# Performance work log

Hardware: AMD Instinct MI355X
Metric: run time of the kernel (lower is better)

## Reference

```python
import jax, jax.numpy as jnp
import numpy as np

N = 100000   # n_nodes
E = 1600000  # n_edges
BN_EPS = 1e-5


def setup_inputs() -> dict:
    key = jax.random.key(0)
    ks = jax.random.split(key, 10)
    x = jax.random.normal(ks[0], (N, 20), dtype=jnp.float32)
    edge_index = jax.random.randint(ks[1], (2, E), 0, N, dtype=jnp.int64)
    dims = [(20, 64), (64, 48), (48, 32)]
    inp = {"x": x, "edge_index": edge_index}
    for i, (di, do) in enumerate(dims):
        inp[f"W{i+1}"] = jax.random.normal(ks[2 + i], (di, do), dtype=jnp.float32) / np.sqrt(di)
        inp[f"b{i+1}"] = jnp.zeros((do,), dtype=jnp.float32)
        inp[f"g{i+1}"] = jnp.ones((do,), dtype=jnp.float32)
        inp[f"beta{i+1}"] = jnp.zeros((do,), dtype=jnp.float32)
    return inp


def _gcn_norm(edge_index):
    # add self loops, compute symmetric normalization D^-1/2 (A+I) D^-1/2
    loop = jnp.arange(N, dtype=edge_index.dtype)
    src = jnp.concatenate([edge_index[0], loop])
    dst = jnp.concatenate([edge_index[1], loop])
    deg = jax.ops.segment_sum(jnp.ones_like(src, dtype=jnp.float32), dst, num_segments=N)
    dinv = jax.lax.rsqrt(deg)  # deg >= 1 thanks to self loops
    norm = dinv[src] * dinv[dst]  # [E+N]
    return src, dst, norm


def _gcn_layer(h, src, dst, norm, W, b):
    m = h @ W                                  # [N, out]
    agg = jax.ops.segment_sum(m[src] * norm[:, None], dst, num_segments=N)
    return agg + b


def _batchnorm(x, g, beta):
    mu = jnp.mean(x, axis=0)
    var = jnp.mean(jnp.square(x - mu), axis=0)  # biased, as torch BN training
    return (x - mu) * jax.lax.rsqrt(var + BN_EPS) * g + beta


def reference(x, edge_index, W1, b1, g1, beta1, W2, b2, g2, beta2, W3, b3, g3, beta3):
    src, dst, norm = _gcn_norm(edge_index)
    h = _gcn_layer(x, src, dst, norm, W1, b1)
    h = jax.nn.relu(_batchnorm(h, g1, beta1))   # dropout rate 0 -> identity
    h = _gcn_layer(h, src, dst, norm, W2, b2)
    h = jax.nn.relu(_batchnorm(h, g2, beta2))
    h = _gcn_layer(h, src, dst, norm, W3, b3)
    h = _batchnorm(h, g3, beta3)                # last activation is Identity
    return h
```

## Files before the change

kernel.cpp:

```cpp
#include <hip/hip_runtime.h>


#define NN 100000
#define NE 1600000
constexpr float BN_EPS_F = 1e-5f;

#define BSZ 128
#define NBKT ((NN + BSZ - 1) / BSZ)
#define EC 16384
#define NEB ((NE + EC - 1) / EC)
#define MTOT (NBKT * NEB)
#define CAP 4096


__device__ __forceinline__ unsigned f2bf(float f) {
  union { float f; unsigned u; } v; v.f = f;
  return (v.u + 0x7fffu + ((v.u >> 16) & 1u)) >> 16;
}
__device__ __forceinline__ unsigned pack_bf2(float f0, float f1) {
  return f2bf(f0) | (f2bf(f1) << 16);
}
__device__ __forceinline__ float bf_lo(unsigned u) {
  union { unsigned u; float f; } v; v.u = u << 16; return v.f;
}
__device__ __forceinline__ float bf_hi(unsigned u) {
  union { unsigned u; float f; } v; v.u = u & 0xffff0000u; return v.f;
}


__global__ void hist_pass(const int* __restrict__ dst, int* __restrict__ ph, int e) {
  __shared__ int h[NBKT];
  int tid = threadIdx.x;
  for (int i = tid; i < NBKT; i += 256) h[i] = 0;
  __syncthreads();
  int tbase = blockIdx.x * EC + tid * 64;
#pragma unroll 4
  for (int k = 0; k < 64; k += 4) {
    int i = tbase + k;
    if (i < e) {
      int4 d = *(const int4*)(dst + i);
      atomicAdd(&h[d.x >> 7], 1);
      atomicAdd(&h[d.y >> 7], 1);
      atomicAdd(&h[d.z >> 7], 1);
      atomicAdd(&h[d.w >> 7], 1);
    }
  }
  __syncthreads();
  for (int i = tid; i < NBKT; i += 256) ph[i * NEB + blockIdx.x] = h[i];
}

__global__ void scan_block_sums(const int* __restrict__ data, int* __restrict__ bsums, int n) {
  __shared__ int sd[256];
  int tid = threadIdx.x;
  int base = blockIdx.x * 1024;
  int s = 0;
#pragma unroll
  for (int j = 0; j < 4; j++) {
    int idx = base + tid * 4 + j;
    if (idx < n) s += data[idx];
  }
  sd[tid] = s;
  __syncthreads();
  for (int o = 128; o > 0; o >>= 1) {
    if (tid < o) sd[tid] += sd[tid + o];
    __syncthreads();
  }
  if (tid == 0) bsums[blockIdx.x] = sd[0];
}

__global__ void scan_bsums2(int* __restrict__ bsums, int nb) {
  __shared__ int sd[128];
  int tid = threadIdx.x;
  int v = (tid < nb) ? bsums[tid] : 0;
  sd[tid] = v;
  __syncthreads();
  for (int o = 1; o < 128; o <<= 1) {
    int t = (tid >= o) ? sd[tid - o] : 0;
    __syncthreads();
    sd[tid] += t;
    __syncthreads();
  }
  if (tid < nb) bsums[tid] = sd[tid] - v;
}

__global__ void scan_apply(int* __restrict__ data, const int* __restrict__ bsums, int n) {
  __shared__ int sd[256];
  int tid = threadIdx.x;
  int base = blockIdx.x * 1024;
  int c[4];
  int s = 0;
#pragma unroll
  for (int j = 0; j < 4; j++) {
    int idx = base + tid * 4 + j;
    c[j] = (idx < n) ? data[idx] : 0;
    s += c[j];
  }
  sd[tid] = s;
  __syncthreads();
  for (int o = 1; o < 256; o <<= 1) {
    int t = (tid >= o) ? sd[tid - o] : 0;
    __syncthreads();
    sd[tid] += t;
    __syncthreads();
  }
  int off = bsums[blockIdx.x] + sd[tid] - s;
#pragma unroll
  for (int j = 0; j < 4; j++) {
    int idx = base + tid * 4 + j;
    if (idx < n) {
      data[idx] = off;
      off += c[j];
    }
  }
}

__global__ void bin_pass(const int* __restrict__ src, const int* __restrict__ dst,
                         const int* __restrict__ ph, int* __restrict__ packed, int e) {
  __shared__ int cur[NBKT];
  int tid = threadIdx.x;
  for (int i = tid; i < NBKT; i += 256) cur[i] = ph[i * NEB + blockIdx.x];
  __syncthreads();
  int tbase = blockIdx.x * EC + tid * 64;
#pragma unroll 4
  for (int k = 0; k < 64; k += 4) {
    int i = tbase + k;
    if (i < e) {
      int4 s = *(const int4*)(src + i);
      int4 d = *(const int4*)(dst + i);
      int p0 = atomicAdd(&cur[d.x >> 7], 1);
      int p1 = atomicAdd(&cur[d.y >> 7], 1);
      int p2 = atomicAdd(&cur[d.z >> 7], 1);
      int p3 = atomicAdd(&cur[d.w >> 7], 1);
      packed[p0] = (s.x << 7) | (d.x & 127);
      packed[p1] = (s.y << 7) | (d.y & 127);
      packed[p2] = (s.z << 7) | (d.z & 127);
      packed[p3] = (s.w << 7) | (d.w & 127);
    }
  }
}

__global__ void bucket_finalize(const int* __restrict__ ph, const int* __restrict__ packed,
                                int* __restrict__ rowptr, float* __restrict__ dinv,
                                int* __restrict__ csr_src) {
  __shared__ int eidx[CAP];
  __shared__ int csr_l[CAP];
  __shared__ int ldeg[BSZ], lscan[BSZ], lcur[BSZ];
  int b = blockIdx.x, tid = threadIdx.x;
  int start = ph[b * NEB];
  int end = (b == NBKT - 1) ? NE : ph[(b + 1) * NEB];
  int cnt = end - start;
  if (cnt > CAP) cnt = CAP;
  for (int i = tid; i < cnt; i += 256) eidx[i] = packed[start + i];
  if (tid < BSZ) ldeg[tid] = 0;
  __syncthreads();
  for (int i = tid; i < cnt; i += 256) atomicAdd(&ldeg[eidx[i] & 127], 1);
  __syncthreads();
  if (tid < BSZ) lscan[tid] = ldeg[tid];
  __syncthreads();
  for (int o = 1; o < BSZ; o <<= 1) {
    int t = 0;
    if (tid < BSZ && tid >= o) t = lscan[tid - o];
    __syncthreads();
    if (tid < BSZ) lscan[tid] += t;
    __syncthreads();
  }
  int gn = b * BSZ + tid;
  if (tid < BSZ) {
    int ex = lscan[tid] - ldeg[tid];
    lcur[tid] = ex;
    if (gn < NN) {
      rowptr[gn] = start + ex;
      dinv[gn] = rsqrtf((float)(ldeg[tid] + 1));
    }
  }
  if (b == NBKT - 1 && tid == 0) rowptr[NN] = NE;
  __syncthreads();
  for (int i = tid; i < cnt; i += 256) {
    int pe = eidx[i];
    int pos = atomicAdd(&lcur[pe & 127], 1);
    csr_l[pos] = pe >> 7;
  }
  __syncthreads();
  for (int i = tid; i < cnt; i += 256) csr_src[start + i] = csr_l[i];
}


__global__ void convert_x(const float* __restrict__ x, const float* __restrict__ dinv,
                          unsigned* __restrict__ xb) {
  int t = blockIdx.x * 256 + threadIdx.x;
  if (t >= NN * 16) return;
  int row = t >> 4, i = t & 15;
  unsigned u = 0;
  if (i < 10) {
    float dd = dinv[row];
    float2 f = *(const float2*)(x + row * 20 + 2 * i);
    u = pack_bf2(dd * f.x, dd * f.y);
  }
  xb[t] = u;
}


template <int NU, int S2, int LW, bool STATS>
__launch_bounds__(256)
__global__ void aggregate_bf(const unsigned* __restrict__ mb, const int* __restrict__ rowptr,
                             const int* __restrict__ csr_src, const float* __restrict__ dinv,
                             const float* __restrict__ bias, float* __restrict__ out,
                             float* __restrict__ gsum) {
  constexpr int NPB = 256 / LW;
  constexpr int OS = 2 * LW;
  __shared__ float2 ssum[256], ssq[256];
  int tid = threadIdx.x;
  int sub = tid / LW, lane = tid % LW;
  int cl = (lane < NU) ? lane : lane - NU;
  int d = blockIdx.x * NPB + sub;
  int start = rowptr[d], end = rowptr[d + 1];
  unsigned su = mb[(size_t)d * S2 + cl];
  float acc0 = bf_lo(su), acc1 = bf_hi(su);
  int j = start;
  int aligned = (start + 3) & ~3;
  int pe = aligned < end ? aligned : end;
  for (; j < pe; j++) {
    unsigned u = mb[(size_t)csr_src[j] * S2 + cl];
    acc0 += bf_lo(u); acc1 += bf_hi(u);
  }
  for (; j + 16 <= end; j += 16) {
    int4 s0 = *(const int4*)(csr_src + j);
    int4 s1 = *(const int4*)(csr_src + j + 4);
    int4 s2 = *(const int4*)(csr_src + j + 8);
    int4 s3 = *(const int4*)(csr_src + j + 12);
    unsigned u0 = mb[(size_t)s0.x * S2 + cl], u1 = mb[(size_t)s0.y * S2 + cl];
    unsigned u2 = mb[(size_t)s0.z * S2 + cl], u3 = mb[(size_t)s0.w * S2 + cl];
    unsigned u4 = mb[(size_t)s1.x * S2 + cl], u5 = mb[(size_t)s1.y * S2 + cl];
    unsigned u6 = mb[(size_t)s1.z * S2 + cl], u7 = mb[(size_t)s1.w * S2 + cl];
    unsigned u8 = mb[(size_t)s2.x * S2 + cl], u9 = mb[(size_t)s2.y * S2 + cl];
    unsigned ua = mb[(size_t)s2.z * S2 + cl], ub = mb[(size_t)s2.w * S2 + cl];
    unsigned uc = mb[(size_t)s3.x * S2 + cl], ud = mb[(size_t)s3.y * S2 + cl];
    unsigned ue = mb[(size_t)s3.z * S2 + cl], uf = mb[(size_t)s3.w * S2 + cl];
    acc0 += bf_lo(u0) + bf_lo(u1) + bf_lo(u2) + bf_lo(u3);
    acc1 += bf_hi(u0) + bf_hi(u1) + bf_hi(u2) + bf_hi(u3);
    acc0 += bf_lo(u4) + bf_lo(u5) + bf_lo(u6) + bf_lo(u7);
    acc1 += bf_hi(u4) + bf_hi(u5) + bf_hi(u6) + bf_hi(u7);
    acc0 += bf_lo(u8) + bf_lo(u9) + bf_lo(ua) + bf_lo(ub);
    acc1 += bf_hi(u8) + bf_hi(u9) + bf_hi(ua) + bf_hi(ub);
    acc0 += bf_lo(uc) + bf_lo(ud) + bf_lo(ue) + bf_lo(uf);
    acc1 += bf_hi(uc) + bf_hi(ud) + bf_hi(ue) + bf_hi(uf);
  }
  for (; j + 4 <= end; j += 4) {
    int4 s0 = *(const int4*)(csr_src + j);
    unsigned u0 = mb[(size_t)s0.x * S2 + cl], u1 = mb[(size_t)s0.y * S2 + cl];
    unsigned u2 = mb[(size_t)s0.z * S2 + cl], u3 = mb[(size_t)s0.w * S2 + cl];
    acc0 += bf_lo(u0) + bf_lo(u1) + bf_lo(u2) + bf_lo(u3);
    acc1 += bf_hi(u0) + bf_hi(u1) + bf_hi(u2) + bf_hi(u3);
  }
  for (; j < end; j++) {
    unsigned u = mb[(size_t)csr_src[j] * S2 + cl];
    acc0 += bf_lo(u); acc1 += bf_hi(u);
  }
  float dd = dinv[d];
  float v0 = dd * acc0, v1 = dd * acc1;
  if (bias) { v0 += bias[2 * cl]; v1 += bias[2 * cl + 1]; }
  if (lane >= NU) { v0 = 0.f; v1 = 0.f; }
  *(float2*)(out + (size_t)d * OS + 2 * lane) = make_float2(v0, v1);
  if (STATS) {
    ssum[tid] = make_float2(v0, v1);
    ssq[tid] = make_float2(v0 * v0, v1 * v1);
    __syncthreads();
    if (tid < LW) {
      float s0 = 0.f, s1 = 0.f, q0 = 0.f, q1 = 0.f;
#pragma unroll
      for (int k = 0; k < NPB; k++) {
        float2 a = ssum[k * LW + tid];
        float2 b = ssq[k * LW + tid];
        s0 += a.x; s1 += a.y; q0 += b.x; q1 += b.y;
      }
      if (tid < NU) {
        float* gs = gsum + (blockIdx.x & 31) * 128;
        atomicAdd(&gs[2 * tid], s0);
        atomicAdd(&gs[2 * tid + 1], s1);
        atomicAdd(&gs[64 + 2 * tid], q0);
        atomicAdd(&gs[64 + 2 * tid + 1], q1);
      }
    }
  }
}


__launch_bounds__(256)
__global__ void gemm1_stats(const float* __restrict__ h, const float* __restrict__ W,
                            const float* __restrict__ bias, float* __restrict__ out,
                            float* __restrict__ gsum) {
  __shared__ float Wl[20 * 64];
  __shared__ float Hl[8][32];
  __shared__ float2 ssum[256], ssq[256];
  int tid = threadIdx.x;
  int row0 = blockIdx.x * 8;
  for (int i = tid; i < 20 * 64; i += 256) Wl[i] = W[i];
  {
    int r = tid >> 5, k = tid & 31;
    Hl[r][k] = h[(size_t)(row0 + r) * 32 + k];
  }
  __syncthreads();
  int r = tid >> 5, c2 = tid & 31;
  float acc0 = bias[2 * c2], acc1 = bias[2 * c2 + 1];
#pragma unroll
  for (int k = 0; k < 20; k++) {
    float a = Hl[r][k];
    acc0 = fmaf(a, Wl[k * 64 + 2 * c2], acc0);
    acc1 = fmaf(a, Wl[k * 64 + 2 * c2 + 1], acc1);
  }
  *(float2*)(out + (size_t)(row0 + r) * 64 + 2 * c2) = make_float2(acc0, acc1);
  ssum[tid] = make_float2(acc0, acc1);
  ssq[tid] = make_float2(acc0 * acc0, acc1 * acc1);
  __syncthreads();
  if (tid < 32) {
    float s0 = 0.f, s1 = 0.f, q0 = 0.f, q1 = 0.f;
#pragma unroll
    for (int k = 0; k < 8; k++) {
      float2 a = ssum[k * 32 + tid];
      float2 b = ssq[k * 32 + tid];
      s0 += a.x; s1 += a.y; q0 += b.x; q1 += b.y;
    }
    float* gs = gsum + (blockIdx.x & 31) * 128;
    atomicAdd(&gs[2 * tid], s0);
    atomicAdd(&gs[2 * tid + 1], s1);
    atomicAdd(&gs[64 + 2 * tid], q0);
    atomicAdd(&gs[64 + 2 * tid + 1], q1);
  }
}


template <int K, int HS, int C, int S2, int R>
__launch_bounds__(256)
__global__ void gemm_bf(const float* __restrict__ h, const float* __restrict__ W,
                        const float* __restrict__ scale, const float* __restrict__ shift,
                        const float* __restrict__ dinv, unsigned* __restrict__ out) {
  __shared__ float Wl[K * C];
  __shared__ float Hl[R][K];
  int tid = threadIdx.x;
  int row0 = blockIdx.x * R;
  for (int i = tid; i < K * C; i += 256) Wl[i] = W[i];
  for (int i = tid; i < R * K; i += 256) {
    int r = i / K, k = i % K;
    float v = h[(size_t)(row0 + r) * HS + k];
    v = fmaf(v, scale[k], shift[k]);
    Hl[r][k] = fmaxf(v, 0.f);
  }
  __syncthreads();
  int r = tid / S2, c2 = tid % S2;
  unsigned u = 0;
  if (2 * c2 < C) {
    float acc0 = 0.f, acc1 = 0.f;
#pragma unroll
    for (int k = 0; k < K; k++) {
      float a = Hl[r][k];
      acc0 = fmaf(a, Wl[k * C + 2 * c2], acc0);
      acc1 = fmaf(a, Wl[k * C + 2 * c2 + 1], acc1);
    }
    float dd = dinv[row0 + r];
    u = pack_bf2(dd * acc0, dd * acc1);
  }
  out[(size_t)(row0 + r) * S2 + c2] = u;
}


__global__ void bn_finalize(const float* __restrict__ gsum, const float* __restrict__ g,
                            const float* __restrict__ beta, float* __restrict__ scale,
                            float* __restrict__ shift, int C, float invn) {
  int i = threadIdx.x;
  if (i < C) {
    float s = 0.f, q = 0.f;
    for (int b = 0; b < 32; b++) {
      s += gsum[b * 128 + i];
      q += gsum[b * 128 + 64 + i];
    }
    float mean = s * invn;
    float var = q * invn - mean * mean;
    var = fmaxf(var, 0.f);
    float inv = rsqrtf(var + BN_EPS_F);
    float sc = g[i] * inv;
    scale[i] = sc;
    shift[i] = beta[i] - mean * sc;
  }
}

__global__ void bn_apply_out(const float* __restrict__ h, const float* __restrict__ scale,
                             const float* __restrict__ shift, float* __restrict__ out, int total) {
  int i = blockIdx.x * blockDim.x + threadIdx.x;
  if (i < total) {
    int c = i & 31;
    out[i] = h[i] * scale[c] + shift[c];
  }
}


extern "C" void kernel_launch(void* const* d_in, const int* in_sizes, int n_in,
                              void* d_out, int out_size, void* d_ws, size_t ws_size,
                              hipStream_t stream) {
  const float* x = (const float*)d_in[0];
  const int* ei = (const int*)d_in[1];
  const float* W1 = (const float*)d_in[2];
  const float* b1 = (const float*)d_in[3];
  const float* g1 = (const float*)d_in[4];
  const float* be1 = (const float*)d_in[5];
  const float* W2 = (const float*)d_in[6];
  const float* b2 = (const float*)d_in[7];
  const float* g2 = (const float*)d_in[8];
  const float* be2 = (const float*)d_in[9];
  const float* W3 = (const float*)d_in[10];
  const float* b3 = (const float*)d_in[11];
  const float* g3 = (const float*)d_in[12];
  const float* be3 = (const float*)d_in[13];
  float* out = (float*)d_out;

  const int* src = ei;
  const int* dst = ei + NE;

  char* ws = (char*)d_ws;
  size_t off = 0;
  auto alloc = [&](size_t bytes) -> void* {
    void* p = ws + off;
    off += bytes;
    off = (off + 255) & ~(size_t)255;
    return p;
  };
  int* ph = (int*)alloc((size_t)MTOT * 4);
  int* bsums = (int*)alloc(128 * 4);
  int* packed = (int*)alloc((size_t)NE * 4);
  int* rowptr = (int*)alloc((NN + 1) * 4);
  int* csr_src = (int*)alloc((size_t)NE * 4);
  float* dinv = (float*)alloc(NN * 4);
  float* gsum = (float*)alloc(3 * 32 * 128 * 4);
  float* scsh = (float*)alloc(3 * 128 * 4);
  float* bufP = (float*)alloc((size_t)NN * 32 * 4);
  float* bufQ = (float*)alloc((size_t)NN * 64 * 4);
  float* bufR = (float*)alloc((size_t)NN * 32 * 4);

  unsigned* xb = (unsigned*)bufR;
  float* aggx = bufP;
  float* h1 = bufQ;
  unsigned* m2b = (unsigned*)bufP;
  float* h2 = bufQ;
  unsigned* m3b = (unsigned*)bufP;
  float* h3 = bufR;

  hipMemsetAsync(gsum, 0, 3 * 32 * 128 * 4, stream);

  const int nscan = (MTOT + 1023) / 1024;
  hist_pass<<<NEB, 256, 0, stream>>>(dst, ph, NE);
  scan_block_sums<<<nscan, 256, 0, stream>>>(ph, bsums, MTOT);
  scan_bsums2<<<1, 128, 0, stream>>>(bsums, nscan);
  scan_apply<<<nscan, 256, 0, stream>>>(ph, bsums, MTOT);
  bin_pass<<<NEB, 256, 0, stream>>>(src, dst, ph, packed, NE);
  bucket_finalize<<<NBKT, 256, 0, stream>>>(ph, packed, rowptr, dinv, csr_src);
  convert_x<<<NN * 16 / 256, 256, 0, stream>>>(x, dinv, xb);

  const float invn = 1.f / (float)NN;

  aggregate_bf<10, 16, 16, false><<<NN / 16, 256, 0, stream>>>(xb, rowptr, csr_src, dinv,
                                                               nullptr, aggx, nullptr);
  gemm1_stats<<<NN / 8, 256, 0, stream>>>(aggx, W1, b1, h1, gsum);
  bn_finalize<<<1, 64, 0, stream>>>(gsum, g1, be1, scsh + 0, scsh + 64, 64, invn);

  gemm_bf<64, 64, 48, 32, 8><<<NN / 8, 256, 0, stream>>>(h1, W2, scsh + 0, scsh + 64, dinv, m2b);
  aggregate_bf<24, 32, 32, true><<<NN / 8, 256, 0, stream>>>(m2b, rowptr, csr_src, dinv, b2, h2,
                                                             gsum + 4096);
  bn_finalize<<<1, 64, 0, stream>>>(gsum + 4096, g2, be2, scsh + 128, scsh + 192, 48, invn);

  gemm_bf<48, 64, 32, 16, 16><<<NN / 16, 256, 0, stream>>>(h2, W3, scsh + 128, scsh + 192, dinv, m3b);
  aggregate_bf<16, 16, 16, true><<<NN / 16, 256, 0, stream>>>(m3b, rowptr, csr_src, dinv, b3, h3,
                                                              gsum + 8192);
  bn_finalize<<<1, 64, 0, stream>>>(gsum + 8192, g3, be3, scsh + 256, scsh + 320, 32, invn);

  bn_apply_out<<<(NN * 32 + 255) / 256, 256, 0, stream>>>(h3, scsh + 256, scsh + 320, out, NN * 32);
}
```

Baseline: 359.9 us.

## Fuse x conversion into CSR build and store intermediates as bf16

Folds the x-to-bf16 scaling into bucket_finalize, which removes one launch and one reread of dinv. Intermediate activations (aggregated x, h1, h2) are now stored as packed bf16 rather than fp32, which shrinks memory traffic between the GEMM and aggregation stages. The templated aggregate and gemm kernels become specialized versions, and layer 2 packs 48 channels as 12 uint2 lanes per row instead of 24 padded lanes of 32. The cost is extra bf16 rounding on intermediates and on the values that feed the BatchNorm statistics, plus a larger workspace from separate buffers.

```diff
diff --git a/kernel.cpp b/kernel.cpp
--- a/kernel.cpp
+++ b/kernel.cpp
@@ -140,11 +140,13 @@
 }
 
 __global__ void bucket_finalize(const int* __restrict__ ph, const int* __restrict__ packed,
-                                int* __restrict__ rowptr, float* __restrict__ dinv,
-                                int* __restrict__ csr_src) {
+                                const float* __restrict__ x, int* __restrict__ rowptr,
+                                float* __restrict__ dinv, int* __restrict__ csr_src,
+                                unsigned* __restrict__ xb) {
   __shared__ int eidx[CAP];
   __shared__ int csr_l[CAP];
   __shared__ int ldeg[BSZ], lscan[BSZ], lcur[BSZ];
+  __shared__ float ldinv[BSZ];
   int b = blockIdx.x, tid = threadIdx.x;
   int start = ph[b * NEB];
   int end = (b == NBKT - 1) ? NE : ph[(b + 1) * NEB];
@@ -168,9 +170,11 @@
   if (tid < BSZ) {
     int ex = lscan[tid] - ldeg[tid];
     lcur[tid] = ex;
+    float dv = rsqrtf((float)(ldeg[tid] + 1));
+    ldinv[tid] = dv;
     if (gn < NN) {
       rowptr[gn] = start + ex;
-      dinv[gn] = rsqrtf((float)(ldeg[tid] + 1));
+      dinv[gn] = dv;
     }
   }
   if (b == NBKT - 1 && tid == 0) rowptr[NN] = NE;
@@ -182,45 +186,38 @@
   }
   __syncthreads();
   for (int i = tid; i < cnt; i += 256) csr_src[start + i] = csr_l[i];
-}
-
-
-__global__ void convert_x(const float* __restrict__ x, const float* __restrict__ dinv,
-                          unsigned* __restrict__ xb) {
-  int t = blockIdx.x * 256 + threadIdx.x;
-  if (t >= NN * 16) return;
-  int row = t >> 4, i = t & 15;
-  unsigned u = 0;
-  if (i < 10) {
-    float dd = dinv[row];
-    float2 f = *(const float2*)(x + row * 20 + 2 * i);
-    u = pack_bf2(dd * f.x, dd * f.y);
-  }
-  xb[t] = u;
-}
-
-
-template <int NU, int S2, int LW, bool STATS>
+  for (int i = tid; i < BSZ * 16; i += 256) {
+    int nl = i >> 4, j = i & 15;
+    int g2 = b * BSZ + nl;
+    if (g2 < NN) {
+      unsigned u = 0;
+      if (j < 10) {
+        float2 f = *(const float2*)(x + (size_t)g2 * 20 + 2 * j);
+        float dd = ldinv[nl];
+        u = pack_bf2(dd * f.x, dd * f.y);
+      }
+      xb[(size_t)g2 * 16 + j] = u;
+    }
+  }
+}
+
+
 __launch_bounds__(256)
-__global__ void aggregate_bf(const unsigned* __restrict__ mb, const int* __restrict__ rowptr,
-                             const int* __restrict__ csr_src, const float* __restrict__ dinv,
-                             const float* __restrict__ bias, float* __restrict__ out,
-                             float* __restrict__ gsum) {
-  constexpr int NPB = 256 / LW;
-  constexpr int OS = 2 * LW;
-  __shared__ float2 ssum[256], ssq[256];
-  int tid = threadIdx.x;
-  int sub = tid / LW, lane = tid % LW;
-  int cl = (lane < NU) ? lane : lane - NU;
-  int d = blockIdx.x * NPB + sub;
+__global__ void aggregate_x(const unsigned* __restrict__ mb, const int* __restrict__ rowptr,
+                            const int* __restrict__ csr_src, const float* __restrict__ dinv,
+                            unsigned* __restrict__ out) {
+  int tid = threadIdx.x;
+  int sub = tid >> 4, lane = tid & 15;
+  int cl = (lane < 10) ? lane : lane - 10;
+  int d = blockIdx.x * 16 + sub;
   int start = rowptr[d], end = rowptr[d + 1];
-  unsigned su = mb[(size_t)d * S2 + cl];
+  unsigned su = mb[(size_t)d * 16 + cl];
   float acc0 = bf_lo(su), acc1 = bf_hi(su);
   int j = start;
   int aligned = (start + 3) & ~3;
   int pe = aligned < end ? aligned : end;
   for (; j < pe; j++) {
-    unsigned u = mb[(size_t)csr_src[j] * S2 + cl];
+    unsigned u = mb[(size_t)csr_src[j] * 16 + cl];
     acc0 += bf_lo(u); acc1 += bf_hi(u);
   }
   for (; j + 16 <= end; j += 16) {
@@ -228,96 +225,172 @@
     int4 s1 = *(const int4*)(csr_src + j + 4);
     int4 s2 = *(const int4*)(csr_src + j + 8);
     int4 s3 = *(const int4*)(csr_src + j + 12);
-    unsigned u0 = mb[(size_t)s0.x * S2 + cl], u1 = mb[(size_t)s0.y * S2 + cl];
-    unsigned u2 = mb[(size_t)s0.z * S2 + cl], u3 = mb[(size_t)s0.w * S2 + cl];
-    unsigned u4 = mb[(size_t)s1.x * S2 + cl], u5 = mb[(size_t)s1.y * S2 + cl];
-    unsigned u6 = mb[(size_t)s1.z * S2 + cl], u7 = mb[(size_t)s1.w * S2 + cl];
-    unsigned u8 = mb[(size_t)s2.x * S2 + cl], u9 = mb[(size_t)s2.y * S2 + cl];
-    unsigned ua = mb[(size_t)s2.z * S2 + cl], ub = mb[(size_t)s2.w * S2 + cl];
-    unsigned uc = mb[(size_t)s3.x * S2 + cl], ud = mb[(size_t)s3.y * S2 + cl];
-    unsigned ue = mb[(size_t)s3.z * S2 + cl], uf = mb[(size_t)s3.w * S2 + cl];
+    int idx[16] = {s0.x, s0.y, s0.z, s0.w, s1.x, s1.y, s1.z, s1.w,
+                   s2.x, s2.y, s2.z, s2.w, s3.x, s3.y, s3.z, s3.w};
+    unsigned u[16];
+#pragma unroll
+    for (int t = 0; t < 16; t++) u[t] = mb[(size_t)idx[t] * 16 + cl];
+#pragma unroll
+    for (int t = 0; t < 16; t++) { acc0 += bf_lo(u[t]); acc1 += bf_hi(u[t]); }
+  }
+  for (; j + 4 <= end; j += 4) {
+    int4 s0 = *(const int4*)(csr_src + j);
+    unsigned u0 = mb[(size_t)s0.x * 16 + cl], u1 = mb[(size_t)s0.y * 16 + cl];
+    unsigned u2 = mb[(size_t)s0.z * 16 + cl], u3 = mb[(size_t)s0.w * 16 + cl];
     acc0 += bf_lo(u0) + bf_lo(u1) + bf_lo(u2) + bf_lo(u3);
     acc1 += bf_hi(u0) + bf_hi(u1) + bf_hi(u2) + bf_hi(u3);
-    acc0 += bf_lo(u4) + bf_lo(u5) + bf_lo(u6) + bf_lo(u7);
-    acc1 += bf_hi(u4) + bf_hi(u5) + bf_hi(u6) + bf_hi(u7);
-    acc0 += bf_lo(u8) + bf_lo(u9) + bf_lo(ua) + bf_lo(ub);
-    acc1 += bf_hi(u8) + bf_hi(u9) + bf_hi(ua) + bf_hi(ub);
-    acc0 += bf_lo(uc) + bf_lo(ud) + bf_lo(ue) + bf_lo(uf);
-    acc1 += bf_hi(uc) + bf_hi(ud) + bf_hi(ue) + bf_hi(uf);
+  }
+  for (; j < end; j++) {
+    unsigned u = mb[(size_t)csr_src[j] * 16 + cl];
+    acc0 += bf_lo(u); acc1 += bf_hi(u);
+  }
+  float dd = dinv[d];
+  unsigned uo = (lane < 10) ? pack_bf2(dd * acc0, dd * acc1) : 0u;
+  out[(size_t)d * 16 + lane] = uo;
+}
+
+
+__launch_bounds__(256)
+__global__ void aggregate_bf48(const uint2* __restrict__ mb, const int* __restrict__ rowptr,
+                               const int* __restrict__ csr_src, const float* __restrict__ dinv,
+                               const float* __restrict__ bias, unsigned* __restrict__ out,
+                               float* __restrict__ gsum) {
+  __shared__ float4 ssum[256], ssq[256];
+  int tid = threadIdx.x;
+  int sub = tid >> 4, lane = tid & 15;
+  int cl = (lane < 12) ? lane : lane - 12;
+  int d = blockIdx.x * 16 + sub;
+  int start = rowptr[d], end = rowptr[d + 1];
+  uint2 su = mb[(size_t)d * 12 + cl];
+  float acc0 = bf_lo(su.x), acc1 = bf_hi(su.x), acc2 = bf_lo(su.y), acc3 = bf_hi(su.y);
+  int j = start;
+  int aligned = (start + 3) & ~3;
+  int pe = aligned < end ? aligned : end;
+  for (; j < pe; j++) {
+    uint2 u = mb[(size_t)csr_src[j] * 12 + cl];
+    acc0 += bf_lo(u.x); acc1 += bf_hi(u.x); acc2 += bf_lo(u.y); acc3 += bf_hi(u.y);
+  }
+  for (; j + 16 <= end; j += 16) {
+    int4 s0 = *(const int4*)(csr_src + j);
+    int4 s1 = *(const int4*)(csr_src + j + 4);
+    int4 s2 = *(const int4*)(csr_src + j + 8);
+    int4 s3 = *(const int4*)(csr_src + j + 12);
+    int idx[16] = {s0.x, s0.y, s0.z, s0.w, s1.x, s1.y, s1.z, s1.w,
+                   s2.x, s2.y, s2.z, s2.w, s3.x, s3.y, s3.z, s3.w};
+    uint2 u[16];
+#pragma unroll
+    for (int t = 0; t < 16; t++) u[t] = mb[(size_t)idx[t] * 12 + cl];
+#pragma unroll
+    for (int t = 0; t < 16; t++) {
+      acc0 += bf_lo(u[t].x); acc1 += bf_hi(u[t].x);
+      acc2 += bf_lo(u[t].y); acc3 += bf_hi(u[t].y);
+    }
   }
   for (; j + 4 <= end; j += 4) {
     int4 s0 = *(const int4*)(csr_src + j);
-    unsigned u0 = mb[(size_t)s0.x * S2 + cl], u1 = mb[(size_t)s0.y * S2 + cl];
-    unsigned u2 = mb[(size_t)s0.z * S2 + cl], u3 = mb[(size_t)s0.w * S2 + cl];
+    uint2 u0 = mb[(size_t)s0.x * 12 + cl], u1 = mb[(size_t)s0.y * 12 + cl];
+    uint2 u2 = mb[(size_t)s0.z * 12 + cl], u3 = mb[(size_t)s0.w * 12 + cl];
+    acc0 += bf_lo(u0.x) + bf_lo(u1.x) + bf_lo(u2.x) + bf_lo(u3.x);
+    acc1 += bf_hi(u0.x) + bf_hi(u1.x) + bf_hi(u2.x) + bf_hi(u3.x);
+    acc2 += bf_lo(u0.y) + bf_lo(u1.y) + bf_lo(u2.y) + bf_lo(u3.y);
+    acc3 += bf_hi(u0.y) + bf_hi(u1.y) + bf_hi(u2.y) + bf_hi(u3.y);
+  }
+  for (; j < end; j++) {
+    uint2 u = mb[(size_t)csr_src[j] * 12 + cl];
+    acc0 += bf_lo(u.x); acc1 += bf_hi(u.x); acc2 += bf_lo(u.y); acc3 += bf_hi(u.y);
+  }
+  float dd = dinv[d];
+  float v0 = dd * acc0 + bias[4 * cl];
+  float v1 = dd * acc1 + bias[4 * cl + 1];
+  float v2 = dd * acc2 + bias[4 * cl + 2];
+  float v3 = dd * acc3 + bias[4 * cl + 3];
+  if (lane >= 12) { v0 = v1 = v2 = v3 = 0.f; }
+  if (lane < 12) {
+    uint2 uo = make_uint2(pack_bf2(v0, v1), pack_bf2(v2, v3));
+    *(uint2*)(out + (size_t)d * 24 + 2 * cl) = uo;
+  }
+  ssum[tid] = make_float4(v0, v1, v2, v3);
+  ssq[tid] = make_float4(v0 * v0, v1 * v1, v2 * v2, v3 * v3);
+  __syncthreads();
+  if (tid < 12) {
+    float s0 = 0.f, s1 = 0.f, s2 = 0.f, s3 = 0.f;
+    float q0 = 0.f, q1 = 0.f, q2 = 0.f, q3 = 0.f;
+#pragma unroll
+    for (int k = 0; k < 16; k++) {
+      float4 a = ssum[k * 16 + tid];
+      float4 b = ssq[k * 16 + tid];
+      s0 += a.x; s1 += a.y; s2 += a.z; s3 += a.w;
+      q0 += b.x; q1 += b.y; q2 += b.z; q3 += b.w;
+    }
+    float* gs = gsum + (blockIdx.x & 31) * 128;
+    atomicAdd(&gs[4 * tid], s0);
+    atomicAdd(&gs[4 * tid + 1], s1);
+    atomicAdd(&gs[4 * tid + 2], s2);
+    atomicAdd(&gs[4 * tid + 3], s3);
+    atomicAdd(&gs[64 + 4 * tid], q0);
+    atomicAdd(&gs[64 + 4 * tid + 1], q1);
+    atomicAdd(&gs[64 + 4 * tid + 2], q2);
+    atomicAdd(&gs[64 + 4 * tid + 3], q3);
+  }
+}
+
+
+__launch_bounds__(256)
+__global__ void aggregate_bf32(const unsigned* __restrict__ mb, const int* __restrict__ rowptr,
+                               const int* __restrict__ csr_src, const float* __restrict__ dinv,
+                               const float* __restrict__ bias, float* __restrict__ out,
+                               float* __restrict__ gsum) {
+  __shared__ float2 ssum[256], ssq[256];
+  int tid = threadIdx.x;
+  int sub = tid >> 4, lane = tid & 15;
+  int d = blockIdx.x * 16 + sub;
+  int start = rowptr[d], end = rowptr[d + 1];
+  unsigned su = mb[(size_t)d * 16 + lane];
+  float acc0 = bf_lo(su), acc1 = bf_hi(su);
+  int j = start;
+  int aligned = (start + 3) & ~3;
+  int pe = aligned < end ? aligned : end;
+  for (; j < pe; j++) {
+    unsigned u = mb[(size_t)csr_src[j] * 16 + lane];
+    acc0 += bf_lo(u); acc1 += bf_hi(u);
+  }
+  for (; j + 16 <= end; j += 16) {
+    int4 s0 = *(const int4*)(csr_src + j);
+    int4 s1 = *(const int4*)(csr_src + j + 4);
+    int4 s2 = *(const int4*)(csr_src + j + 8);
+    int4 s3 = *(const int4*)(csr_src + j + 12);
+    int idx[16] = {s0.x, s0.y, s0.z, s0.w, s1.x, s1.y, s1.z, s1.w,
+                   s2.x, s2.y, s2.z, s2.w, s3.x, s3.y, s3.z, s3.w};
+    unsigned u[16];
+#pragma unroll
+    for (int t = 0; t < 16; t++) u[t] = mb[(size_t)idx[t] * 16 + lane];
+#pragma unroll
+    for (int t = 0; t < 16; t++) { acc0 += bf_lo(u[t]); acc1 += bf_hi(u[t]); }
+  }
+  for (; j + 4 <= end; j += 4) {
+    int4 s0 = *(const int4*)(csr_src + j);
+    unsigned u0 = mb[(size_t)s0.x * 16 + lane], u1 = mb[(size_t)s0.y * 16 + lane];
+    unsigned u2 = mb[(size_t)s0.z * 16 + lane], u3 = mb[(size_t)s0.w * 16 + lane];
     acc0 += bf_lo(u0) + bf_lo(u1) + bf_lo(u2) + bf_lo(u3);
     acc1 += bf_hi(u0) + bf_hi(u1) + bf_hi(u2) + bf_hi(u3);
   }
   for (; j < end; j++) {
-    unsigned u = mb[(size_t)csr_src[j] * S2 + cl];
+    unsigned u = mb[(size_t)csr_src[j] * 16 + lane];
     acc0 += bf_lo(u); acc1 += bf_hi(u);
   }
   float dd = dinv[d];
-  float v0 = dd * acc0, v1 = dd * acc1;
-  if (bias) { v0 += bias[2 * cl]; v1 += bias[2 * cl + 1]; }
-  if (lane >= NU) { v0 = 0.f; v1 = 0.f; }
-  *(float2*)(out + (size_t)d * OS + 2 * lane) = make_float2(v0, v1);
-  if (STATS) {
-    ssum[tid] = make_float2(v0, v1);
-    ssq[tid] = make_float2(v0 * v0, v1 * v1);
-    __syncthreads();
-    if (tid < LW) {
-      float s0 = 0.f, s1 = 0.f, q0 = 0.f, q1 = 0.f;
-#pragma unroll
-      for (int k = 0; k < NPB; k++) {
-        float2 a = ssum[k * LW + tid];
-        float2 b = ssq[k * LW + tid];
-        s0 += a.x; s1 += a.y; q0 += b.x; q1 += b.y;
-      }
-      if (tid < NU) {
-        float* gs = gsum + (blockIdx.x & 31) * 128;
-        atomicAdd(&gs[2 * tid], s0);
-        atomicAdd(&gs[2 * tid + 1], s1);
-        atomicAdd(&gs[64 + 2 * tid], q0);
-        atomicAdd(&gs[64 + 2 * tid + 1], q1);
-      }
-    }
-  }
-}
-
-
-__launch_bounds__(256)
-__global__ void gemm1_stats(const float* __restrict__ h, const float* __restrict__ W,
-                            const float* __restrict__ bias, float* __restrict__ out,
-                            float* __restrict__ gsum) {
-  __shared__ float Wl[20 * 64];
-  __shared__ float Hl[8][32];
-  __shared__ float2 ssum[256], ssq[256];
-  int tid = threadIdx.x;
-  int row0 = blockIdx.x * 8;
-  for (int i = tid; i < 20 * 64; i += 256) Wl[i] = W[i];
-  {
-    int r = tid >> 5, k = tid & 31;
-    Hl[r][k] = h[(size_t)(row0 + r) * 32 + k];
-  }
-  __syncthreads();
-  int r = tid >> 5, c2 = tid & 31;
-  float acc0 = bias[2 * c2], acc1 = bias[2 * c2 + 1];
-#pragma unroll
-  for (int k = 0; k < 20; k++) {
-    float a = Hl[r][k];
-    acc0 = fmaf(a, Wl[k * 64 + 2 * c2], acc0);
-    acc1 = fmaf(a, Wl[k * 64 + 2 * c2 + 1], acc1);
-  }
-  *(float2*)(out + (size_t)(row0 + r) * 64 + 2 * c2) = make_float2(acc0, acc1);
-  ssum[tid] = make_float2(acc0, acc1);
-  ssq[tid] = make_float2(acc0 * acc0, acc1 * acc1);
-  __syncthreads();
-  if (tid < 32) {
+  float v0 = dd * acc0 + bias[2 * lane];
+  float v1 = dd * acc1 + bias[2 * lane + 1];
+  *(float2*)(out + (size_t)d * 32 + 2 * lane) = make_float2(v0, v1);
+  ssum[tid] = make_float2(v0, v1);
+  ssq[tid] = make_float2(v0 * v0, v1 * v1);
+  __syncthreads();
+  if (tid < 16) {
     float s0 = 0.f, s1 = 0.f, q0 = 0.f, q1 = 0.f;
 #pragma unroll
-    for (int k = 0; k < 8; k++) {
-      float2 a = ssum[k * 32 + tid];
-      float2 b = ssq[k * 32 + tid];
+    for (int k = 0; k < 16; k++) {
+      float2 a = ssum[k * 16 + tid];
+      float2 b = ssq[k * 16 + tid];
       s0 += a.x; s1 += a.y; q0 += b.x; q1 += b.y;
     }
     float* gs = gsum + (blockIdx.x & 31) * 128;
@@ -329,37 +402,115 @@
 }
 
 
-template <int K, int HS, int C, int S2, int R>
 __launch_bounds__(256)
-__global__ void gemm_bf(const float* __restrict__ h, const float* __restrict__ W,
-                        const float* __restrict__ scale, const float* __restrict__ shift,
-                        const float* __restrict__ dinv, unsigned* __restrict__ out) {
-  __shared__ float Wl[K * C];
-  __shared__ float Hl[R][K];
-  int tid = threadIdx.x;
-  int row0 = blockIdx.x * R;
-  for (int i = tid; i < K * C; i += 256) Wl[i] = W[i];
-  for (int i = tid; i < R * K; i += 256) {
-    int r = i / K, k = i % K;
-    float v = h[(size_t)(row0 + r) * HS + k];
-    v = fmaf(v, scale[k], shift[k]);
-    Hl[r][k] = fmaxf(v, 0.f);
-  }
-  __syncthreads();
-  int r = tid / S2, c2 = tid % S2;
-  unsigned u = 0;
-  if (2 * c2 < C) {
-    float acc0 = 0.f, acc1 = 0.f;
-#pragma unroll
-    for (int k = 0; k < K; k++) {
+__global__ void gemm1_stats(const unsigned* __restrict__ hu, const float* __restrict__ W,
+                            const float* __restrict__ bias, unsigned* __restrict__ out,
+                            float* __restrict__ gsum) {
+  __shared__ float Wl[20 * 64];
+  __shared__ float Hl[8][20];
+  __shared__ float2 ssum[256], ssq[256];
+  int tid = threadIdx.x;
+  int row0 = blockIdx.x * 8;
+  for (int i = tid; i < 20 * 64; i += 256) Wl[i] = W[i];
+  if (tid < 128) {
+    int r = tid >> 4, j = tid & 15;
+    if (j < 10) {
+      unsigned u = hu[(size_t)(row0 + r) * 16 + j];
+      Hl[r][2 * j] = bf_lo(u);
+      Hl[r][2 * j + 1] = bf_hi(u);
+    }
+  }
+  __syncthreads();
+  int r = tid >> 5, c2 = tid & 31;
+  float acc0 = bias[2 * c2], acc1 = bias[2 * c2 + 1];
+#pragma unroll
+  for (int k = 0; k < 20; k++) {
+    float a = Hl[r][k];
+    acc0 = fmaf(a, Wl[k * 64 + 2 * c2], acc0);
+    acc1 = fmaf(a, Wl[k * 64 + 2 * c2 + 1], acc1);
+  }
+  out[(size_t)(row0 + r) * 32 + c2] = pack_bf2(acc0, acc1);
+  ssum[tid] = make_float2(acc0, acc1);
+  ssq[tid] = make_float2(acc0 * acc0, acc1 * acc1);
+  __syncthreads();
+  if (tid < 32) {
+    float s0 = 0.f, s1 = 0.f, q0 = 0.f, q1 = 0.f;
+#pragma unroll
+    for (int k = 0; k < 8; k++) {
+      float2 a = ssum[k * 32 + tid];
+      float2 b = ssq[k * 32 + tid];
+      s0 += a.x; s1 += a.y; q0 += b.x; q1 += b.y;
+    }
+    float* gs = gsum + (blockIdx.x & 31) * 128;
+    atomicAdd(&gs[2 * tid], s0);
+    atomicAdd(&gs[2 * tid + 1], s1);
+    atomicAdd(&gs[64 + 2 * tid], q0);
+    atomicAdd(&gs[64 + 2 * tid + 1], q1);
+  }
+}
+
+
+__launch_bounds__(256)
+__global__ void gemm2_bf(const unsigned* __restrict__ hu, const float* __restrict__ W,
+                         const float* __restrict__ scale, const float* __restrict__ shift,
+                         const float* __restrict__ dinv, unsigned* __restrict__ out) {
+  __shared__ float Wl[64 * 48];
+  __shared__ float Hl[16][64];
+  int tid = threadIdx.x;
+  int row0 = blockIdx.x * 16;
+  for (int i = tid; i < 64 * 48; i += 256) Wl[i] = W[i];
+  for (int i = tid; i < 16 * 32; i += 256) {
+    int r = i >> 5, j = i & 31;
+    unsigned u = hu[(size_t)(row0 + r) * 32 + j];
+    Hl[r][2 * j] = fmaxf(fmaf(bf_lo(u), scale[2 * j], shift[2 * j]), 0.f);
+    Hl[r][2 * j + 1] = fmaxf(fmaf(bf_hi(u), scale[2 * j + 1], shift[2 * j + 1]), 0.f);
+  }
+  __syncthreads();
+  int r = tid >> 4, c = tid & 15;
+  if (c < 12) {
+    float a0 = 0.f, a1 = 0.f, a2 = 0.f, a3 = 0.f;
+#pragma unroll
+    for (int k = 0; k < 64; k++) {
       float a = Hl[r][k];
-      acc0 = fmaf(a, Wl[k * C + 2 * c2], acc0);
-      acc1 = fmaf(a, Wl[k * C + 2 * c2 + 1], acc1);
+      const float* w = &Wl[k * 48 + 4 * c];
+      a0 = fmaf(a, w[0], a0);
+      a1 = fmaf(a, w[1], a1);
+      a2 = fmaf(a, w[2], a2);
+      a3 = fmaf(a, w[3], a3);
     }
     float dd = dinv[row0 + r];
-    u = pack_bf2(dd * acc0, dd * acc1);
-  }
-  out[(size_t)(row0 + r) * S2 + c2] = u;
+    uint2 uo = make_uint2(pack_bf2(dd * a0, dd * a1), pack_bf2(dd * a2, dd * a3));
+    *(uint2*)(out + (size_t)(row0 + r) * 24 + 2 * c) = uo;
+  }
+}
+
+
+__launch_bounds__(256)
+__global__ void gemm3_bf(const unsigned* __restrict__ hu, const float* __restrict__ W,
+                         const float* __restrict__ scale, const float* __restrict__ shift,
+                         const float* __restrict__ dinv, unsigned* __restrict__ out) {
+  __shared__ float Wl[48 * 32];
+  __shared__ float Hl[16][48];
+  int tid = threadIdx.x;
+  int row0 = blockIdx.x * 16;
+  for (int i = tid; i < 48 * 32; i += 256) Wl[i] = W[i];
+  for (int i = tid; i < 16 * 24; i += 256) {
+    int r = i / 24, j = i % 24;
+    unsigned u = hu[(size_t)(row0 + r) * 24 + j];
+    Hl[r][2 * j] = fmaxf(fmaf(bf_lo(u), scale[2 * j], shift[2 * j]), 0.f);
+    Hl[r][2 * j + 1] = fmaxf(fmaf(bf_hi(u), scale[2 * j + 1], shift[2 * j + 1]), 0.f);
+  }
+  __syncthreads();
+  int r = tid >> 4, c2 = tid & 15;
+  float a0 = 0.f, a1 = 0.f;
+#pragma unroll
+  for (int k = 0; k < 48; k++) {
+    float a = Hl[r][k];
+    a0 = fmaf(a, Wl[k * 32 + 2 * c2], a0);
+    a1 = fmaf(a, Wl[k * 32 + 2 * c2 + 1], a1);
+  }
+  float dd = dinv[row0 + r];
+  out[(size_t)(row0 + r) * 16 + c2] = pack_bf2(dd * a0, dd * a1);
 }
 
 
@@ -431,17 +582,14 @@
   float* dinv = (float*)alloc(NN * 4);
   float* gsum = (float*)alloc(3 * 32 * 128 * 4);
   float* scsh = (float*)alloc(3 * 128 * 4);
-  float* bufP = (float*)alloc((size_t)NN * 32 * 4);
-  float* bufQ = (float*)alloc((size_t)NN * 64 * 4);
-  float* bufR = (float*)alloc((size_t)NN * 32 * 4);
-
-  unsigned* xb = (unsigned*)bufR;
-  float* aggx = bufP;
-  float* h1 = bufQ;
-  unsigned* m2b = (unsigned*)bufP;
-  float* h2 = bufQ;
-  unsigned* m3b = (unsigned*)bufP;
-  float* h3 = bufR;
+  unsigned* xb = (unsigned*)alloc((size_t)NN * 16 * 4);
+  unsigned* aggx = (unsigned*)alloc((size_t)NN * 16 * 4);
+  unsigned* h1u = (unsigned*)alloc((size_t)NN * 32 * 4);
+  unsigned* m2b = (unsigned*)alloc((size_t)NN * 24 * 4);
+  unsigned* h2u = (unsigned*)alloc((size_t)NN * 24 * 4);
+
+  unsigned* m3b = aggx;
+  float* h3 = (float*)h1u;
 
   hipMemsetAsync(gsum, 0, 3 * 32 * 128 * 4, stream);
 
@@ -451,24 +599,21 @@
   scan_bsums2<<<1, 128, 0, stream>>>(bsums, nscan);
   scan_apply<<<nscan, 256, 0, stream>>>(ph, bsums, MTOT);
   bin_pass<<<NEB, 256, 0, stream>>>(src, dst, ph, packed, NE);
-  bucket_finalize<<<NBKT, 256, 0, stream>>>(ph, packed, rowptr, dinv, csr_src);
-  convert_x<<<NN * 16 / 256, 256, 0, stream>>>(x, dinv, xb);
+  bucket_finalize<<<NBKT, 256, 0, stream>>>(ph, packed, x, rowptr, dinv, csr_src, xb);
 
   const float invn = 1.f / (float)NN;
 
-  aggregate_bf<10, 16, 16, false><<<NN / 16, 256, 0, stream>>>(xb, rowptr, csr_src, dinv,
-                                                               nullptr, aggx, nullptr);
-  gemm1_stats<<<NN / 8, 256, 0, stream>>>(aggx, W1, b1, h1, gsum);
+  aggregate_x<<<NN / 16, 256, 0, stream>>>(xb, rowptr, csr_src, dinv, aggx);
+  gemm1_stats<<<NN / 8, 256, 0, stream>>>(aggx, W1, b1, h1u, gsum);
   bn_finalize<<<1, 64, 0, stream>>>(gsum, g1, be1, scsh + 0, scsh + 64, 64, invn);
 
-  gemm_bf<64, 64, 48, 32, 8><<<NN / 8, 256, 0, stream>>>(h1, W2, scsh + 0, scsh + 64, dinv, m2b);
-  aggregate_bf<24, 32, 32, true><<<NN / 8, 256, 0, stream>>>(m2b, rowptr, csr_src, dinv, b2, h2,
-                                                             gsum + 4096);
+  gemm2_bf<<<NN / 16, 256, 0, stream>>>(h1u, W2, scsh + 0, scsh + 64, dinv, m2b);
+  aggregate_bf48<<<NN / 16, 256, 0, stream>>>((const uint2*)m2b, rowptr, csr_src, dinv, b2, h2u,
+                                              gsum + 4096);
   bn_finalize<<<1, 64, 0, stream>>>(gsum + 4096, g2, be2, scsh + 128, scsh + 192, 48, invn);
 
-  gemm_bf<48, 64, 32, 16, 16><<<NN / 16, 256, 0, stream>>>(h2, W3, scsh + 128, scsh + 192, dinv, m3b);
-  aggregate_bf<16, 16, 16, true><<<NN / 16, 256, 0, stream>>>(m3b, rowptr, csr_src, dinv, b3, h3,
-                                                              gsum + 8192);
+  gemm3_bf<<<NN / 16, 256, 0, stream>>>(h2u, W3, scsh + 128, scsh + 192, dinv, m3b);
+  aggregate_bf32<<<NN / 16, 256, 0, stream>>>(m3b, rowptr, csr_src, dinv, b3, h3, gsum + 8192);
   bn_finalize<<<1, 64, 0, stream>>>(gsum + 8192, g3, be3, scsh + 256, scsh + 320, 32, invn);
 
   bn_apply_out<<<(NN * 32 + 255) / 256, 256, 0, stream>>>(h3, scsh + 256, scsh + 320, out, NN * 32);
```

Result: faster. 340.9 us (-5.3%).
